# Kernel optimization log

Measured on AMD Instinct MI355X. Metric: run time of the kernel, lower is better.

The kernel has to match this reference:

```python
import jax, jax.numpy as jnp
import numpy as np

NUM_NODES = 100000
PROP_STEP = 8


def _spmm(vals, rows, cols, x):
    # sparse [N,N] @ dense [N,F]: gather source rows, scale, scatter-add to dest
    gathered = x[cols] * vals[:, None]  # [E, F]
    return jax.ops.segment_sum(gathered, rows, num_segments=NUM_NODES)


def setup_inputs() -> dict:
    key = jax.random.key(0)
    k1, k2, k3, k4, k5 = jax.random.split(key, 5)
    N, E, C = NUM_NODES, 3200000, 128
    x = jax.random.normal(k1, (N, C), dtype=jnp.float32)
    # xavier_uniform for weight [c_in, c_out]
    limit = float(np.sqrt(6.0 / (C + C)))
    weight = jax.random.uniform(k2, (C, C), dtype=jnp.float32, minval=-limit, maxval=limit)
    lap_vals = jax.random.uniform(k3, (E,), dtype=jnp.float32)
    lap_rows = jax.random.randint(k4, (E,), 0, N, dtype=jnp.int64)
    lap_cols = jax.random.randint(k5, (E,), 0, N, dtype=jnp.int64)
    return {"x": x, "weight": weight, "lap_vals": lap_vals,
            "lap_rows": lap_rows, "lap_cols": lap_cols}


def reference(x, weight, lap_vals, lap_rows, lap_cols):
    # filter_type='low', dropout inactive (eval / p=0)
    identity = x
    out = x @ weight  # [N, c_out]
    for _ in range(PROP_STEP):
        out = _spmm(lap_vals, lap_rows, lap_cols, out)
    return identity + out
```

## Files before the change

kernel.cpp:

```cpp
#include <hip/hip_runtime.h>
#include <hip/hip_bf16.h>
#include <hip/hip_fp16.h>
#include <stdint.h>

#define CCH 128
#define FINAL_SCALE 268435456.0f
#define RND 2048
#define BUKSH 9
#define BUKROWS 512
#define MAXBUK 256


__global__ void hist_kernel(const int* __restrict__ rows, int* __restrict__ counts, int E) {
    int stride = gridDim.x * blockDim.x;
    for (int e = blockIdx.x * blockDim.x + threadIdx.x; e < E; e += stride)
        atomicAdd(&counts[rows[e]], 1);
}

__global__ __launch_bounds__(1024) void scanA_kernel(const int* __restrict__ counts,
                                                     int* __restrict__ row_ptr,
                                                     int* __restrict__ partials, int n) {
    __shared__ int tile[1024];
    int t = threadIdx.x;
    int i = blockIdx.x * 1024 + t;
    tile[t] = (i < n) ? counts[i] : 0;
    __syncthreads();
    for (int off = 1; off < 1024; off <<= 1) {
        int add = (t >= off) ? tile[t - off] : 0;
        __syncthreads();
        tile[t] += add;
        __syncthreads();
    }
    if (i < n) row_ptr[i + 1] = tile[t];
    if (t == 1023) partials[blockIdx.x] = tile[1023];
}

__global__ __launch_bounds__(1024) void scanB_kernel(int* __restrict__ partials,
                                                     int* __restrict__ row_ptr, int nb) {
    __shared__ int tile[1024];
    int t = threadIdx.x;
    tile[t] = (t < nb) ? partials[t] : 0;
    __syncthreads();
    for (int off = 1; off < 1024; off <<= 1) {
        int add = (t >= off) ? tile[t - off] : 0;
        __syncthreads();
        tile[t] += add;
        __syncthreads();
    }
    if (t < nb) partials[t] = (t == 0) ? 0 : tile[t - 1];
    if (t == 0) row_ptr[0] = 0;
}

__global__ void scanC_kernel(const int* __restrict__ partials, int* __restrict__ row_ptr, int n) {
    int i = blockIdx.x * blockDim.x + threadIdx.x;
    if (i < n) row_ptr[i + 1] += partials[i >> 10];
}

__global__ void gcur_init_kernel(const int* __restrict__ row_ptr, int* __restrict__ gcur,
                                 int nbuk, int n) {
    int b = threadIdx.x;
    if (b < nbuk) {
        int r = b << BUKSH;
        gcur[b] = row_ptr[r < n ? r : n];
    }
}

__global__ __launch_bounds__(256) void part_kernel(const int* __restrict__ rows,
                                                   const int* __restrict__ cols,
                                                   const float* __restrict__ vals,
                                                   int* __restrict__ gcur,
                                                   int4* __restrict__ recs,
                                                   int E, int nbuk) {
    __shared__ int hist[MAXBUK];
    __shared__ int offs[MAXBUK];
    __shared__ int cur[MAXBUK];
    __shared__ int gbase[MAXBUK];
    __shared__ int4 stage[RND];

    int base = blockIdx.x * RND;
    int cnt = E - base;
    if (cnt > RND) cnt = RND;
    if (cnt <= 0) return;

    for (int i = threadIdx.x; i < nbuk; i += 256) hist[i] = 0;
    __syncthreads();

    int myr[RND / 256], myc[RND / 256];
    float myv[RND / 256];
#pragma unroll
    for (int k = 0; k < RND / 256; ++k) {
        int li = k * 256 + threadIdx.x;
        bool ok = li < cnt;
        int gi = base + li;
        myr[k] = ok ? rows[gi] : -1;
        myc[k] = ok ? cols[gi] : 0;
        myv[k] = ok ? vals[gi] : 0.f;
        if (ok) atomicAdd(&hist[myr[k] >> BUKSH], 1);
    }
    __syncthreads();

    if (threadIdx.x == 0) {
        int run = 0;
        for (int b = 0; b < nbuk; ++b) {
            offs[b] = run;
            cur[b] = run;
            run += hist[b];
        }
    }
    __syncthreads();
    if (threadIdx.x < nbuk) gbase[threadIdx.x] = atomicAdd(&gcur[threadIdx.x], hist[threadIdx.x]);
    __syncthreads();

#pragma unroll
    for (int k = 0; k < RND / 256; ++k) {
        if (myr[k] >= 0) {
            int b = myr[k] >> BUKSH;
            int p = atomicAdd(&cur[b], 1);
            stage[p] = make_int4(myr[k], myc[k], __float_as_int(myv[k]), 0);
        }
    }
    __syncthreads();

    for (int i = threadIdx.x; i < cnt; i += 256) {
        int4 r = stage[i];
        int b = r.x >> BUKSH;
        recs[(size_t)gbase[b] + (i - offs[b])] = r;
    }
}

__global__ __launch_bounds__(512) void csrfill_kernel(const int4* __restrict__ recs,
                                                      const int* __restrict__ row_ptr,
                                                      int2* __restrict__ edges,
                                                      int n) {
    __shared__ int lfill[BUKROWS];
    int bucket = blockIdx.x;
    int r0 = bucket << BUKSH;
    int r1 = r0 + BUKROWS;
    if (r0 >= n) return;
    if (r1 > n) r1 = n;
    for (int i = threadIdx.x; i < BUKROWS; i += 512) lfill[i] = 0;
    __syncthreads();
    int bstart = row_ptr[r0];
    int bend = row_ptr[r1];
    int i = bstart + threadIdx.x;
    for (; i + 512 < bend; i += 1024) {
        int4 a = recs[i];
        int4 b = recs[i + 512];
        int pa = row_ptr[a.x] + atomicAdd(&lfill[a.x - r0], 1);
        int pb = row_ptr[b.x] + atomicAdd(&lfill[b.x - r0], 1);
        edges[pa] = make_int2(a.y, a.z);
        edges[pb] = make_int2(b.y, b.z);
    }
    if (i < bend) {
        int4 a = recs[i];
        int pa = row_ptr[a.x] + atomicAdd(&lfill[a.x - r0], 1);
        edges[pa] = make_int2(a.y, a.z);
    }
}


#define GEMM_ROWS 64

__global__ __launch_bounds__(256) void gemm_kernel(const float* __restrict__ x,
                                                   const float* __restrict__ w,
                                                   __half* __restrict__ out, int n) {
    __shared__ __half2 wl[CCH * 64];
    for (int i = threadIdx.x; i < CCH * 64 / 2; i += 256) {
        float4 v = ((const float4*)w)[i];
        wl[2 * i]     = __float22half2_rn(make_float2(v.x, v.y));
        wl[2 * i + 1] = __float22half2_rn(make_float2(v.z, v.w));
    }
    __syncthreads();

    int tc = threadIdx.x & 31;
    int tr = threadIdx.x >> 5;
    int rbase = blockIdx.x * GEMM_ROWS + tr * 8;
    int nr = n - rbase;
    if (nr > 8) nr = 8;
    if (nr <= 0) nr = 0;

    float acc[8][4] = {};
    const float* xp = x + (size_t)rbase * CCH;

    float4 xc[8];
#pragma unroll
    for (int j = 0; j < 8; ++j)
        xc[j] = (j < nr) ? *(const float4*)(xp + (size_t)j * CCH)
                         : make_float4(0.f, 0.f, 0.f, 0.f);

    for (int k = 0; k < CCH; k += 4) {
        float4 xn[8];
        if (k + 4 < CCH) {
#pragma unroll
            for (int j = 0; j < 8; ++j)
                xn[j] = (j < nr) ? *(const float4*)(xp + (size_t)j * CCH + k + 4)
                                 : make_float4(0.f, 0.f, 0.f, 0.f);
        }
#pragma unroll
        for (int kk = 0; kk < 4; ++kk) {
            __half2 w01 = wl[(k + kk) * 64 + tc * 2];
            __half2 w23 = wl[(k + kk) * 64 + tc * 2 + 1];
            float2 f01 = __half22float2(w01);
            float2 f23 = __half22float2(w23);
#pragma unroll
            for (int j = 0; j < 8; ++j) {
                float xs = (kk == 0) ? xc[j].x : (kk == 1) ? xc[j].y : (kk == 2) ? xc[j].z : xc[j].w;
                acc[j][0] += xs * f01.x;
                acc[j][1] += xs * f01.y;
                acc[j][2] += xs * f23.x;
                acc[j][3] += xs * f23.y;
            }
        }
        if (k + 4 < CCH) {
#pragma unroll
            for (int j = 0; j < 8; ++j) xc[j] = xn[j];
        }
    }
#pragma unroll
    for (int j = 0; j < 8; ++j)
        if (j < nr) {
            __half2* orow = (__half2*)(out + (size_t)(rbase + j) * CCH + tc * 4);
            orow[0] = __float22half2_rn(make_float2(acc[j][0], acc[j][1]));
            orow[1] = __float22half2_rn(make_float2(acc[j][2], acc[j][3]));
        }
}


template <int FINAL>
__global__ __launch_bounds__(256) void spmm_kernel(const int* __restrict__ row_ptr,
                                                   const int2* __restrict__ edges,
                                                   const __half* __restrict__ src,
                                                   __half* __restrict__ dsth,
                                                   float* __restrict__ dstf,
                                                   const float* __restrict__ identity,
                                                   int n) {
    int lane = threadIdx.x & 63;
    int row = (blockIdx.x * blockDim.x + threadIdx.x) >> 6;
    if (row >= n) return;
    int g = lane >> 4;
    int gl = lane & 15;

    int s = row_ptr[row];
    int e = row_ptr[row + 1];

    float acc[8] = {};

    for (int base = s; base < e; base += 16) {
        int2 ed[4];
        float4 gv[4];
#pragma unroll
        for (int t = 0; t < 4; ++t) {
            int idx = base + g * 4 + t;
            bool ok = idx < e;
            ed[t] = edges[ok ? idx : s];
            if (!ok) ed[t].y = 0;
        }
#pragma unroll
        for (int t = 0; t < 4; ++t)
            gv[t] = *(const float4*)(src + (size_t)ed[t].x * CCH + gl * 8);
#pragma unroll
        for (int t = 0; t < 4; ++t) {
            float v = __int_as_float(ed[t].y);
            const __half* h = (const __half*)&gv[t];
#pragma unroll
            for (int j = 0; j < 8; ++j)
                acc[j] += v * __half2float(h[j]);
        }
    }

#pragma unroll
    for (int j = 0; j < 8; ++j) {
        acc[j] += __shfl_xor(acc[j], 16, 64);
        acc[j] += __shfl_xor(acc[j], 32, 64);
    }

    if (FINAL) {
        if (g == 0) {
            const float* iv = identity + (size_t)row * CCH + gl * 8;
            float4 o;
            o.x = iv[0] + acc[0] * FINAL_SCALE;
            o.y = iv[1] + acc[1] * FINAL_SCALE;
            o.z = iv[2] + acc[2] * FINAL_SCALE;
            o.w = iv[3] + acc[3] * FINAL_SCALE;
            *(float4*)(dstf + (size_t)row * CCH + gl * 8) = o;
        } else if (g == 1) {
            const float* iv = identity + (size_t)row * CCH + gl * 8 + 4;
            float4 o;
            o.x = iv[0] + acc[4] * FINAL_SCALE;
            o.y = iv[1] + acc[5] * FINAL_SCALE;
            o.z = iv[2] + acc[6] * FINAL_SCALE;
            o.w = iv[3] + acc[7] * FINAL_SCALE;
            *(float4*)(dstf + (size_t)row * CCH + gl * 8 + 4) = o;
        }
    } else {
        if (g == 0) {
            __half2 h[4];
            h[0] = __float22half2_rn(make_float2(acc[0] * 0.0625f, acc[1] * 0.0625f));
            h[1] = __float22half2_rn(make_float2(acc[2] * 0.0625f, acc[3] * 0.0625f));
            h[2] = __float22half2_rn(make_float2(acc[4] * 0.0625f, acc[5] * 0.0625f));
            h[3] = __float22half2_rn(make_float2(acc[6] * 0.0625f, acc[7] * 0.0625f));
            *(float4*)(dsth + (size_t)row * CCH + gl * 8) = *(float4*)h;
        }
    }
}


static inline size_t align256(size_t x) { return (x + 255) & ~(size_t)255; }

extern "C" void kernel_launch(void* const* d_in, const int* in_sizes, int n_in,
                              void* d_out, int out_size, void* d_ws, size_t ws_size,
                              hipStream_t stream) {
    const float* x = (const float*)d_in[0];
    const float* w = (const float*)d_in[1];
    const float* lap_vals = (const float*)d_in[2];
    const int* lap_rows = (const int*)d_in[3];
    const int* lap_cols = (const int*)d_in[4];

    const int N = in_sizes[0] / CCH;
    const int E = in_sizes[2];
    const int NB = (N + 1023) / 1024;
    const int NBUK = (N + BUKROWS - 1) >> BUKSH;

    char* ws = (char*)d_ws;
    size_t off = 0;
    __half* bufA = (__half*)(ws + off); off = align256(off + (size_t)N * CCH * sizeof(__half));
    __half* bufB = (__half*)(ws + off); off = align256(off + (size_t)N * CCH * sizeof(__half));
    int2* edges = (int2*)(ws + off);    off = align256(off + (size_t)E * sizeof(int2));
    int* row_ptr = (int*)(ws + off);    off = align256(off + (size_t)(N + 1) * sizeof(int));
    int* counts = (int*)(ws + off);     off = align256(off + (size_t)N * sizeof(int));
    int* partials = (int*)(ws + off);   off = align256(off + (size_t)NB * sizeof(int));
    int* gcur = (int*)(ws + off);       off = align256(off + (size_t)MAXBUK * sizeof(int));
    (void)ws_size;
    int4* recs = (int4*)bufA;

    float* out = (float*)d_out;

    hipMemsetAsync(counts, 0, (size_t)N * sizeof(int), stream);

    hist_kernel<<<2048, 256, 0, stream>>>(lap_rows, counts, E);
    scanA_kernel<<<NB, 1024, 0, stream>>>(counts, row_ptr, partials, N);
    scanB_kernel<<<1, 1024, 0, stream>>>(partials, row_ptr, NB);
    scanC_kernel<<<(N + 255) / 256, 256, 0, stream>>>(partials, row_ptr, N);
    gcur_init_kernel<<<1, MAXBUK, 0, stream>>>(row_ptr, gcur, NBUK, N);
    part_kernel<<<(E + RND - 1) / RND, 256, 0, stream>>>(lap_rows, lap_cols, lap_vals,
                                                         gcur, recs, E, NBUK);
    csrfill_kernel<<<NBUK, 512, 0, stream>>>(recs, row_ptr, edges, N);

    gemm_kernel<<<(N + GEMM_ROWS - 1) / GEMM_ROWS, 256, 0, stream>>>(x, w, bufA, N);

    int spmm_blocks = (N + 3) / 4;
    const __half* src = bufA;
    __half* dst = bufB;
    for (int step = 1; step <= 7; ++step) {
        spmm_kernel<0><<<spmm_blocks, 256, 0, stream>>>(row_ptr, edges, src, dst, nullptr, nullptr, N);
        __half* t = (__half*)src;
        src = dst;
        dst = t;
    }
    spmm_kernel<1><<<spmm_blocks, 256, 0, stream>>>(row_ptr, edges, src, nullptr, out, x, N);
}
```

Before: 1.266 ms.

## Build CSR row pointers per bucket instead of global per-row histogram and scan

Replaces the global per-row histogram (3.2M global atomics) and the three-kernel prefix scan with a bucket-level histogram in shared memory plus a tiny serial bucket scan. Per-row counts and offsets are then computed inside the CSR fill kernel from the bucket's records, using a shared-memory scan. This cuts global atomic traffic and kernel launches in the preprocessing phase, at the cost of an extra pass over the records in csrfill.

New measurement: 1.159 ms. 8.5% less time.

```diff
diff --git a/kernel.cpp b/kernel.cpp
--- a/kernel.cpp
+++ b/kernel.cpp
@@ -11,57 +11,30 @@
 #define MAXBUK 256
 
 
-__global__ void hist_kernel(const int* __restrict__ rows, int* __restrict__ counts, int E) {
+__global__ __launch_bounds__(256) void bucket_hist_kernel(const int* __restrict__ rows,
+                                                          int* __restrict__ bukcnt,
+                                                          int E, int nbuk) {
+    __shared__ int h[MAXBUK];
+    for (int i = threadIdx.x; i < nbuk; i += 256) h[i] = 0;
+    __syncthreads();
     int stride = gridDim.x * blockDim.x;
     for (int e = blockIdx.x * blockDim.x + threadIdx.x; e < E; e += stride)
-        atomicAdd(&counts[rows[e]], 1);
-}
-
-__global__ __launch_bounds__(1024) void scanA_kernel(const int* __restrict__ counts,
-                                                     int* __restrict__ row_ptr,
-                                                     int* __restrict__ partials, int n) {
-    __shared__ int tile[1024];
-    int t = threadIdx.x;
-    int i = blockIdx.x * 1024 + t;
-    tile[t] = (i < n) ? counts[i] : 0;
-    __syncthreads();
-    for (int off = 1; off < 1024; off <<= 1) {
-        int add = (t >= off) ? tile[t - off] : 0;
-        __syncthreads();
-        tile[t] += add;
-        __syncthreads();
-    }
-    if (i < n) row_ptr[i + 1] = tile[t];
-    if (t == 1023) partials[blockIdx.x] = tile[1023];
-}
-
-__global__ __launch_bounds__(1024) void scanB_kernel(int* __restrict__ partials,
-                                                     int* __restrict__ row_ptr, int nb) {
-    __shared__ int tile[1024];
-    int t = threadIdx.x;
-    tile[t] = (t < nb) ? partials[t] : 0;
-    __syncthreads();
-    for (int off = 1; off < 1024; off <<= 1) {
-        int add = (t >= off) ? tile[t - off] : 0;
-        __syncthreads();
-        tile[t] += add;
-        __syncthreads();
-    }
-    if (t < nb) partials[t] = (t == 0) ? 0 : tile[t - 1];
-    if (t == 0) row_ptr[0] = 0;
-}
-
-__global__ void scanC_kernel(const int* __restrict__ partials, int* __restrict__ row_ptr, int n) {
-    int i = blockIdx.x * blockDim.x + threadIdx.x;
-    if (i < n) row_ptr[i + 1] += partials[i >> 10];
-}
-
-__global__ void gcur_init_kernel(const int* __restrict__ row_ptr, int* __restrict__ gcur,
-                                 int nbuk, int n) {
-    int b = threadIdx.x;
-    if (b < nbuk) {
-        int r = b << BUKSH;
-        gcur[b] = row_ptr[r < n ? r : n];
+        atomicAdd(&h[rows[e] >> BUKSH], 1);
+    __syncthreads();
+    for (int i = threadIdx.x; i < nbuk; i += 256)
+        if (h[i]) atomicAdd(&bukcnt[i], h[i]);
+}
+
+__global__ void bucket_scan_kernel(const int* __restrict__ bukcnt, int* __restrict__ bukptr,
+                                   int* __restrict__ gcur, int nbuk) {
+    if (threadIdx.x == 0) {
+        int run = 0;
+        for (int b = 0; b < nbuk; ++b) {
+            bukptr[b] = run;
+            gcur[b] = run;
+            run += bukcnt[b];
+        }
+        bukptr[nbuk] = run;
     }
 }
 
@@ -128,32 +101,59 @@
     }
 }
 
-__global__ __launch_bounds__(512) void csrfill_kernel(const int4* __restrict__ recs,
-                                                      const int* __restrict__ row_ptr,
-                                                      int2* __restrict__ edges,
-                                                      int n) {
+__global__ __launch_bounds__(512) void csrfill2_kernel(const int4* __restrict__ recs,
+                                                       const int* __restrict__ bukptr,
+                                                       int* __restrict__ row_ptr,
+                                                       int2* __restrict__ edges,
+                                                       int n, int E) {
+    __shared__ int lcnt[BUKROWS];
+    __shared__ int lscan[BUKROWS];
     __shared__ int lfill[BUKROWS];
     int bucket = blockIdx.x;
     int r0 = bucket << BUKSH;
-    int r1 = r0 + BUKROWS;
     if (r0 >= n) return;
-    if (r1 > n) r1 = n;
-    for (int i = threadIdx.x; i < BUKROWS; i += 512) lfill[i] = 0;
-    __syncthreads();
-    int bstart = row_ptr[r0];
-    int bend = row_ptr[r1];
-    int i = bstart + threadIdx.x;
+    int t = threadIdx.x;
+    int bstart = bukptr[bucket];
+    int bend = bukptr[bucket + 1];
+
+    lcnt[t] = 0;
+    __syncthreads();
+
+    for (int i = bstart + t; i < bend; i += 512)
+        atomicAdd(&lcnt[recs[i].x - r0], 1);
+    __syncthreads();
+
+    int v = lcnt[t];
+    lscan[t] = v;
+    __syncthreads();
+    for (int off = 1; off < 512; off <<= 1) {
+        int add = (t >= off) ? lscan[t - off] : 0;
+        __syncthreads();
+        lscan[t] += add;
+        __syncthreads();
+    }
+    int excl = lscan[t] - v;
+
+    int r = r0 + t;
+    if (r < n) row_ptr[r] = bstart + excl;
+    if (bucket == 0 && t == 0) row_ptr[n] = E;
+
+    lfill[t] = 0;
+    lcnt[t] = bstart + excl;
+    __syncthreads();
+
+    int i = bstart + t;
     for (; i + 512 < bend; i += 1024) {
         int4 a = recs[i];
         int4 b = recs[i + 512];
-        int pa = row_ptr[a.x] + atomicAdd(&lfill[a.x - r0], 1);
-        int pb = row_ptr[b.x] + atomicAdd(&lfill[b.x - r0], 1);
+        int pa = lcnt[a.x - r0] + atomicAdd(&lfill[a.x - r0], 1);
+        int pb = lcnt[b.x - r0] + atomicAdd(&lfill[b.x - r0], 1);
         edges[pa] = make_int2(a.y, a.z);
         edges[pb] = make_int2(b.y, b.z);
     }
     if (i < bend) {
         int4 a = recs[i];
-        int pa = row_ptr[a.x] + atomicAdd(&lfill[a.x - r0], 1);
+        int pa = lcnt[a.x - r0] + atomicAdd(&lfill[a.x - r0], 1);
         edges[pa] = make_int2(a.y, a.z);
     }
 }
@@ -318,7 +318,6 @@
 
     const int N = in_sizes[0] / CCH;
     const int E = in_sizes[2];
-    const int NB = (N + 1023) / 1024;
     const int NBUK = (N + BUKROWS - 1) >> BUKSH;
 
     char* ws = (char*)d_ws;
@@ -327,24 +326,21 @@
     __half* bufB = (__half*)(ws + off); off = align256(off + (size_t)N * CCH * sizeof(__half));
     int2* edges = (int2*)(ws + off);    off = align256(off + (size_t)E * sizeof(int2));
     int* row_ptr = (int*)(ws + off);    off = align256(off + (size_t)(N + 1) * sizeof(int));
-    int* counts = (int*)(ws + off);     off = align256(off + (size_t)N * sizeof(int));
-    int* partials = (int*)(ws + off);   off = align256(off + (size_t)NB * sizeof(int));
+    int* bukcnt = (int*)(ws + off);     off = align256(off + (size_t)MAXBUK * sizeof(int));
+    int* bukptr = (int*)(ws + off);     off = align256(off + (size_t)(MAXBUK + 1) * sizeof(int));
     int* gcur = (int*)(ws + off);       off = align256(off + (size_t)MAXBUK * sizeof(int));
     (void)ws_size;
     int4* recs = (int4*)bufA;
 
     float* out = (float*)d_out;
 
-    hipMemsetAsync(counts, 0, (size_t)N * sizeof(int), stream);
-
-    hist_kernel<<<2048, 256, 0, stream>>>(lap_rows, counts, E);
-    scanA_kernel<<<NB, 1024, 0, stream>>>(counts, row_ptr, partials, N);
-    scanB_kernel<<<1, 1024, 0, stream>>>(partials, row_ptr, NB);
-    scanC_kernel<<<(N + 255) / 256, 256, 0, stream>>>(partials, row_ptr, N);
-    gcur_init_kernel<<<1, MAXBUK, 0, stream>>>(row_ptr, gcur, NBUK, N);
+    hipMemsetAsync(bukcnt, 0, (size_t)MAXBUK * sizeof(int), stream);
+
+    bucket_hist_kernel<<<512, 256, 0, stream>>>(lap_rows, bukcnt, E, NBUK);
+    bucket_scan_kernel<<<1, 64, 0, stream>>>(bukcnt, bukptr, gcur, NBUK);
     part_kernel<<<(E + RND - 1) / RND, 256, 0, stream>>>(lap_rows, lap_cols, lap_vals,
                                                          gcur, recs, E, NBUK);
-    csrfill_kernel<<<NBUK, 512, 0, stream>>>(recs, row_ptr, edges, N);
+    csrfill2_kernel<<<NBUK, 512, 0, stream>>>(recs, bukptr, row_ptr, edges, N, E);
 
     gemm_kernel<<<(N + GEMM_ROWS - 1) / GEMM_ROWS, 256, 0, stream>>>(x, w, bufA, N);
 
```
